# Kernel optimization log

Measured on AMD Instinct MI355X. Metric: run time of the kernel, lower is better.

## Reference

```python
import jax, jax.numpy as jnp
import numpy as np

IN_F = 4096
OUT_F = 4096
R_BLOCKS = 4
D = IN_F // R_BLOCKS          # 1024 block size
NUM_TASKS = 5
POOL = 5
EPS0 = 1e-05
SEQ = 4096


def setup_inputs() -> dict:
    key = jax.random.key(0)
    k1, k2, k3, k4 = jax.random.split(key, 4)
    return {
        "input": jax.random.normal(k1, (1, SEQ, IN_F), jnp.float32),
        "lora_route": jax.random.normal(k2, (NUM_TASKS, IN_F, POOL), jnp.float32) * 0.02,
        "lora_down": jax.random.normal(k3, (NUM_TASKS, R_BLOCKS, D, D), jnp.float32) * 0.01,
        "W": jax.random.normal(k4, (OUT_F, IN_F), jnp.float32) * 0.02,
        "task_id": 5,
    }


def _block_diag(Q):
    # Q: [r, d, d] -> [r*d, r*d] block-diagonal
    r, d, _ = Q.shape
    out = jnp.zeros((r * d, r * d), Q.dtype)
    for i in range(r):
        out = out.at[i * d:(i + 1) * d, i * d:(i + 1) * d].set(Q[i])
    return out


def reference(input, lora_route, lora_down, W, task_id):
    # eval-mode forward of OFTInjectedLinear (block_share=False, is_coft=True)
    n_tasks, in_f, pool = lora_route.shape
    r, d = lora_down.shape[1], lora_down.shape[2]
    # project_batch: eps = (eps0 * d * d) / sqrt(r)
    eps = jnp.asarray(EPS0 * d * d, input.dtype) / jnp.sqrt(jnp.asarray(r, input.dtype))

    route = lora_route[task_id - 1][None]                     # [1, in, pool]
    input_mean = jnp.mean(input, axis=1, keepdims=True)       # [1, 1, in]
    omegas = jax.nn.softmax(jnp.matmul(input_mean, route), axis=2)  # [1, 1, pool]
    omegas_mean = jnp.mean(omegas, axis=(0, 1))[:task_id]     # [task_id]
    k = min(task_id, 2)
    _, I_idx = jax.lax.top_k(omegas_mean, k)                  # selected tasks

    eye_d = jnp.eye(d, dtype=input.dtype)
    delta = jnp.eye(in_f, dtype=input.dtype)
    for i in range(k):                                        # k is a small static int
        j = I_idx[i]
        R = jnp.take(lora_down, j, axis=0)                    # [r, d, d]
        # COFT projection toward the ZERO matrix (source uses torch.zeros for I)
        nrm = jnp.sqrt(jnp.sum(R * R, axis=(1, 2), keepdims=True))  # per-block fro norm
        Rp = jnp.where(nrm <= eps, R, eps * R / jnp.maximum(nrm, 1e-12))
        # batched Cayley: Q = (I - skew) (I + skew)^{-1}
        skew = 0.5 * (Rp - jnp.swapaxes(Rp, 1, 2))
        Q = jnp.matmul(eye_d - skew, jnp.linalg.inv(eye_d + skew))  # [r, d, d]
        bd = _block_diag(Q)                                   # [in, in]
        omega_j = omegas[0, 0, j]                             # scalar (B==1)
        delta = delta * (omega_j * bd)                        # ELEMENTWISE, as in source

    filt = jnp.matmul(delta, W.T)                             # [in, out]
    return jnp.matmul(input, filt)                            # [1, S, out]
```

## Files before the change

kernel.cpp:

```cpp
#include <hip/hip_runtime.h>
#include <stdint.h>


typedef __bf16 bf16;
typedef __bf16 bf16x4 __attribute__((ext_vector_type(4)));
typedef __bf16 bf16x8 __attribute__((ext_vector_type(8)));
typedef float  f32x4  __attribute__((ext_vector_type(4)));

#define AS1 __attribute__((address_space(1)))
#define AS3 __attribute__((address_space(3)))

constexpr size_t OFF_INBF = 0;
constexpr size_t OFF_WV   = OFF_INBF + (size_t)4096 * 4096 * 2;
constexpr size_t OFF_MEAN = OFF_WV + (size_t)4096 * 4096 * 2;
constexpr size_t OFF_T    = OFF_MEAN + 4096 * 4;
constexpr size_t OFF_NRM2 = OFF_T + 8 * 1024 * 4;
constexpr size_t OFF_INFO = OFF_NRM2 + 64;
constexpr size_t OFF_V    = OFF_INFO + 64;

__global__ void mean_cvt(const float4* __restrict__ in4, float* __restrict__ meansum,
                         bf16* __restrict__ ob) {
    const int t  = threadIdx.x;
    const int f4 = blockIdx.x * 256 + t;
    const int s0 = blockIdx.y * 32;
    float sx = 0.f, sy = 0.f, sz = 0.f, sw = 0.f;
    for (int s = s0; s < s0 + 32; ++s) {
        float4 vx = in4[(size_t)s * 1024 + f4];
        sx += vx.x; sy += vx.y; sz += vx.z; sw += vx.w;
        bf16x4 bv;
        bv[0] = (bf16)vx.x; bv[1] = (bf16)vx.y; bv[2] = (bf16)vx.z; bv[3] = (bf16)vx.w;
        *(bf16x4*)&ob[(size_t)s * 4096 + f4 * 4] = bv;
    }
    atomicAdd(&meansum[f4 * 4 + 0], sx);
    atomicAdd(&meansum[f4 * 4 + 1], sy);
    atomicAdd(&meansum[f4 * 4 + 2], sz);
    atomicAdd(&meansum[f4 * 4 + 3], sw);
}

__global__ void omega_kernel(const float* __restrict__ meansum, const float* __restrict__ lora_route,
                             const int* __restrict__ task_id_p, int* __restrict__ info_i,
                             float* __restrict__ info_f) {
    __shared__ float red[256];
    __shared__ float logits[5];
    const int t = threadIdx.x;
    const int tid = task_id_p[0];
    const float* route = lora_route + (size_t)(tid - 1) * 4096 * 5;
    float acc[5] = {0.f, 0.f, 0.f, 0.f, 0.f};
    for (int f = t; f < 4096; f += 256) {
        float m = meansum[f] * (1.0f / 4096.0f);
#pragma unroll
        for (int p = 0; p < 5; ++p) acc[p] += m * route[f * 5 + p];
    }
    for (int p = 0; p < 5; ++p) {
        red[t] = acc[p];
        __syncthreads();
        for (int s = 128; s > 0; s >>= 1) {
            if (t < s) red[t] += red[t + s];
            __syncthreads();
        }
        if (t == 0) logits[p] = red[0];
        __syncthreads();
    }
    if (t == 0) {
        float mx = logits[0];
        for (int p = 1; p < 5; ++p) mx = fmaxf(mx, logits[p]);
        float e[5], se = 0.f;
        for (int p = 0; p < 5; ++p) { e[p] = expf(logits[p] - mx); se += e[p]; }
        float om[5];
        for (int p = 0; p < 5; ++p) om[p] = e[p] / se;
        const int n = tid < 5 ? tid : 5;
        int j1 = 0;
        for (int p = 1; p < n; ++p) if (om[p] > om[j1]) j1 = p;
        int j2 = -1;
        for (int p = 0; p < n; ++p) if (p != j1 && (j2 < 0 || om[p] > om[j2])) j2 = p;
        const int k = tid < 2 ? tid : 2;
        info_i[0] = j1;
        info_i[1] = (k > 1) ? j2 : j1;
        info_i[2] = k;
        float c = om[j1];
        if (k > 1) c *= om[j2];
        info_f[3] = c;
    }
}

__global__ void diag_kernel(const float* __restrict__ lora_down, const int* __restrict__ info_i,
                            float* __restrict__ T, float* __restrict__ nrm2) {
    const int bid = blockIdx.x;
    const int ts = bid >> 6;
    const int rb = (bid >> 4) & 3;
    const int a  = bid & 15;
    const int k = info_i[2];
    if (ts >= k) return;
    const int j = info_i[ts];
    const float* R = lora_down + ((size_t)(j * 4 + rb) << 20);
    __shared__ float X[64][65];
    __shared__ float Y[64][65];
    const int t = threadIdx.x;
    const int i = t >> 2, g = t & 3;
    const int a64 = a * 64;
    float tacc = 0.f, nacc = 0.f;
    for (int b = 0; b < 16; ++b) {
        __syncthreads();
#pragma unroll
        for (int qq = 0; qq < 4; ++qq) {
            const int fi = qq * 256 + t;
            const int row = fi >> 4, c4 = fi & 15;
            float4 vx = *(const float4*)&R[(size_t)(a64 + row) * 1024 + b * 64 + c4 * 4];
            X[row][c4 * 4 + 0] = vx.x; X[row][c4 * 4 + 1] = vx.y;
            X[row][c4 * 4 + 2] = vx.z; X[row][c4 * 4 + 3] = vx.w;
            nacc += vx.x * vx.x + vx.y * vx.y + vx.z * vx.z + vx.w * vx.w;
            float4 vy = *(const float4*)&R[(size_t)(b * 64 + row) * 1024 + a64 + c4 * 4];
            Y[row][c4 * 4 + 0] = vy.x; Y[row][c4 * 4 + 1] = vy.y;
            Y[row][c4 * 4 + 2] = vy.z; Y[row][c4 * 4 + 3] = vy.w;
        }
        __syncthreads();
#pragma unroll
        for (int s = 0; s < 16; ++s) {
            float xv = X[i][g * 16 + s];
            float yv = Y[g * 16 + s][i];
            float d = xv - yv;
            tacc += d * d;
        }
    }
    tacc += __shfl_xor(tacc, 1);
    tacc += __shfl_xor(tacc, 2);
    if (g == 0) T[((ts * 4 + rb) << 10) + a64 + i] = tacc;
    for (int off = 32; off > 0; off >>= 1) nacc += __shfl_down(nacc, off);
    if ((t & 63) == 0) atomicAdd(&nrm2[ts * 4 + rb], nacc);
}

__global__ void vbuild(const float* __restrict__ T, const float* __restrict__ nrm2,
                       const int* __restrict__ info_i, const float* __restrict__ info_f,
                       float* __restrict__ v) {
    const int i = blockIdx.x * 256 + threadIdx.x;
    const int k = info_i[2];
    const float c = info_f[3];
    const int rb = i >> 10, di = i & 1023;
    const float eps = 1e-5f * 1024.0f * 1024.0f / 2.0f;
    float q = c;
    for (int ts = 0; ts < k; ++ts) {
        float nrm = sqrtf(nrm2[ts * 4 + rb]);
        float scale = (nrm <= eps) ? 1.0f : eps / fmaxf(nrm, 1e-12f);
        q *= 1.0f - 0.5f * scale * scale * T[((ts * 4 + rb) << 10) + di];
    }
    v[i] = q;
}

__global__ void scaleW(const float4* __restrict__ W4, const float* __restrict__ v,
                       bf16* __restrict__ Wv) {
    const size_t stride = (size_t)gridDim.x * blockDim.x;
    for (size_t i = (size_t)blockIdx.x * blockDim.x + threadIdx.x; i < (size_t)4096 * 1024; i += stride) {
        float4 w = W4[i];
        const float* vp = &v[(i & 1023) << 2];
        bf16x4 o;
        o[0] = (bf16)(w.x * vp[0]);
        o[1] = (bf16)(w.y * vp[1]);
        o[2] = (bf16)(w.z * vp[2]);
        o[3] = (bf16)(w.w * vp[3]);
        *(bf16x4*)&Wv[i << 2] = o;
    }
}

__device__ __forceinline__ void gload_lds16(const bf16* g, bf16* lds) {
    __builtin_amdgcn_global_load_lds((const AS1 void*)g, (AS3 void*)lds, 16, 0, 0);
}

__global__ __launch_bounds__(512, 2) void gemm256(const bf16* __restrict__ A,
                                                  const bf16* __restrict__ B,
                                                  float* __restrict__ C) {
    __shared__ bf16 lds[65536];
    const int t = threadIdx.x;
    const int w = t >> 6, l = t & 63;
    const int bid = blockIdx.x;
    const int swz = ((bid & 7) << 5) | (bid >> 3);
    const int bm = swz >> 4, bn = swz & 15;
    const int wm = w >> 2, wn = w & 3;
    const int rl = l & 15, q = l >> 4;
    const int xm = (l & 7) << 4;

    const int srow = (w << 4) + (l >> 3);
    const int scol = ((l & 7) ^ (l >> 3)) << 3;
    const bf16* pA = A + (size_t)((bm << 8) + srow) * 4096 + scol;
    const bf16* pB = B + (size_t)((bn << 8) + srow) * 4096 + scol;

#define STG(dstE, srcP, h, kt) do {                                                          \
        gload_lds16((srcP) + (size_t)((h) * 128) * 4096 + (size_t)(kt) * 64,                 \
                    (bf16*)&lds[(dstE) + (h) * 8192 + w * 1024]);                            \
        gload_lds16((srcP) + (size_t)((h) * 128 + 8) * 4096 + (size_t)(kt) * 64,             \
                    (bf16*)&lds[(dstE) + (h) * 8192 + w * 1024 + 512]);                      \
    } while (0)

    const int aB = (((wm << 7) + rl) << 6);
    const int bB = 16384 + (((wn << 6) + rl) << 6);
    const int c0 = (((q << 4) + 0) ^ xm) >> 1;
    const int c1 = (((q << 4) + 64) ^ xm) >> 1;

    f32x4 acc[8][4] = {};

    STG(0, pA, 0, 0); STG(0, pA, 1, 0);
    STG(16384, pB, 0, 0); STG(16384, pB, 1, 0);
    STG(32768, pA, 0, 1); STG(32768, pA, 1, 1);

    for (int kt = 0; kt < 64; ++kt) {
        const int bufE = (kt & 1) << 15;
        const int nb = bufE ^ 32768;
        if (kt < 63) asm volatile("s_waitcnt vmcnt(4)" ::: "memory");
        else         asm volatile("s_waitcnt vmcnt(0)" ::: "memory");
        __builtin_amdgcn_s_barrier();
        asm volatile("" ::: "memory");

        bf16x8 a0[8], b0[4], a1[8], b1[4];
#pragma unroll
        for (int m = 0; m < 8; ++m) a0[m] = *(const bf16x8*)&lds[bufE + aB + m * 1024 + c0];
#pragma unroll
        for (int n = 0; n < 4; ++n) b0[n] = *(const bf16x8*)&lds[bufE + bB + n * 1024 + c0];
        if (kt + 1 < 64) STG(nb + 16384, pB, 0, kt + 1);
        __builtin_amdgcn_s_setprio(1);
#pragma unroll
        for (int m = 0; m < 4; ++m)
#pragma unroll
            for (int n = 0; n < 4; ++n)
                acc[m][n] = __builtin_amdgcn_mfma_f32_16x16x32_bf16(a0[m], b0[n], acc[m][n], 0, 0, 0);
        __builtin_amdgcn_s_setprio(0);
        __builtin_amdgcn_s_barrier();

#pragma unroll
        for (int m = 0; m < 8; ++m) a1[m] = *(const bf16x8*)&lds[bufE + aB + m * 1024 + c1];
#pragma unroll
        for (int n = 0; n < 4; ++n) b1[n] = *(const bf16x8*)&lds[bufE + bB + n * 1024 + c1];
        if (kt + 1 < 64) STG(nb + 16384, pB, 1, kt + 1);
        __builtin_amdgcn_s_setprio(1);
#pragma unroll
        for (int m = 4; m < 8; ++m)
#pragma unroll
            for (int n = 0; n < 4; ++n)
                acc[m][n] = __builtin_amdgcn_mfma_f32_16x16x32_bf16(a0[m], b0[n], acc[m][n], 0, 0, 0);
        __builtin_amdgcn_s_setprio(0);
        asm volatile("s_waitcnt lgkmcnt(0)" ::: "memory");
        __builtin_amdgcn_s_barrier();

        if (kt + 2 < 64) STG(bufE, pA, 0, kt + 2);
        __builtin_amdgcn_s_setprio(1);
#pragma unroll
        for (int m = 0; m < 4; ++m)
#pragma unroll
            for (int n = 0; n < 4; ++n)
                acc[m][n] = __builtin_amdgcn_mfma_f32_16x16x32_bf16(a1[m], b1[n], acc[m][n], 0, 0, 0);
        __builtin_amdgcn_s_setprio(0);
        __builtin_amdgcn_s_barrier();

        if (kt + 2 < 64) STG(bufE, pA, 1, kt + 2);
        __builtin_amdgcn_s_setprio(1);
#pragma unroll
        for (int m = 4; m < 8; ++m)
#pragma unroll
            for (int n = 0; n < 4; ++n)
                acc[m][n] = __builtin_amdgcn_mfma_f32_16x16x32_bf16(a1[m], b1[n], acc[m][n], 0, 0, 0);
        __builtin_amdgcn_s_setprio(0);
    }
#undef STG

    const int crow = (bm << 8) + (wm << 7) + (q << 2);
    const int ccol = (bn << 8) + (wn << 6) + rl;
#pragma unroll
    for (int m = 0; m < 8; ++m)
#pragma unroll
        for (int n = 0; n < 4; ++n)
#pragma unroll
            for (int r = 0; r < 4; ++r)
                C[(size_t)(crow + m * 16 + r) * 4096 + ccol + n * 16] = acc[m][n][r];
}

extern "C" void kernel_launch(void* const* d_in, const int* in_sizes, int n_in,
                              void* d_out, int out_size, void* d_ws, size_t ws_size,
                              hipStream_t stream) {
    const float* input      = (const float*)d_in[0];
    const float* lora_route = (const float*)d_in[1];
    const float* lora_down  = (const float*)d_in[2];
    const float* W          = (const float*)d_in[3];
    const int*   task_id    = (const int*)d_in[4];

    char* ws = (char*)d_ws;
    bf16*  inbf    = (bf16*)(ws + OFF_INBF);
    bf16*  Wv      = (bf16*)(ws + OFF_WV);
    float* meansum = (float*)(ws + OFF_MEAN);
    float* T       = (float*)(ws + OFF_T);
    float* nrm2    = (float*)(ws + OFF_NRM2);
    int*   info_i  = (int*)(ws + OFF_INFO);
    float* info_f  = (float*)(ws + OFF_INFO);
    float* v       = (float*)(ws + OFF_V);
    float* out     = (float*)d_out;

    hipMemsetAsync(ws + OFF_MEAN, 0, OFF_V + 4096 * 4 - OFF_MEAN, stream);

    mean_cvt<<<dim3(4, 128), 256, 0, stream>>>((const float4*)input, meansum, inbf);
    omega_kernel<<<1, 256, 0, stream>>>(meansum, lora_route, task_id, info_i, info_f);
    diag_kernel<<<128, 256, 0, stream>>>(lora_down, info_i, T, nrm2);
    vbuild<<<16, 256, 0, stream>>>(T, nrm2, info_i, info_f, v);
    scaleW<<<4096, 256, 0, stream>>>((const float4*)W, v, Wv);
    gemm256<<<256, 512, 0, stream>>>(inbf, Wv, out);
}
```

Measured before the change: 210.8 us.

## Widen grids for mean and diag kernels and deepen GEMM B-tile prefetch

mean_cvt now uses four times more blocks, each covering fewer sequence rows. diag_kernel is split across 2048 blocks that each handle one 64x64 tile pair and combine results with atomics. Both changes aim to fill more compute units during these memory-bound preprocessing kernels. The GEMM main loop is rescheduled so B tiles are prefetched one step further ahead, with more barriers and lgkmcnt waits interleaved to overlap LDS reads with MFMA. This adds atomic traffic and extra synchronisation, and the new vmcnt counts must match the reordered loads to stay correct.

After: 334.1 us. +58.5%, slower.

```diff
diff --git a/kernel.cpp b/kernel.cpp
--- a/kernel.cpp
+++ b/kernel.cpp
@@ -22,9 +22,9 @@
                          bf16* __restrict__ ob) {
     const int t  = threadIdx.x;
     const int f4 = blockIdx.x * 256 + t;
-    const int s0 = blockIdx.y * 32;
+    const int s0 = blockIdx.y * 8;
     float sx = 0.f, sy = 0.f, sz = 0.f, sw = 0.f;
-    for (int s = s0; s < s0 + 32; ++s) {
+    for (int s = s0; s < s0 + 8; ++s) {
         float4 vx = in4[(size_t)s * 1024 + f4];
         sx += vx.x; sy += vx.y; sz += vx.z; sw += vx.w;
         bf16x4 bv;
@@ -86,9 +86,10 @@
 __global__ void diag_kernel(const float* __restrict__ lora_down, const int* __restrict__ info_i,
                             float* __restrict__ T, float* __restrict__ nrm2) {
     const int bid = blockIdx.x;
-    const int ts = bid >> 6;
-    const int rb = (bid >> 4) & 3;
-    const int a  = bid & 15;
+    const int ts = bid >> 10;
+    const int rb = (bid >> 8) & 3;
+    const int a  = (bid >> 4) & 15;
+    const int b  = bid & 15;
     const int k = info_i[2];
     if (ts >= k) return;
     const int j = info_i[ts];
@@ -97,34 +98,30 @@
     __shared__ float Y[64][65];
     const int t = threadIdx.x;
     const int i = t >> 2, g = t & 3;
-    const int a64 = a * 64;
-    float tacc = 0.f, nacc = 0.f;
-    for (int b = 0; b < 16; ++b) {
-        __syncthreads();
-#pragma unroll
-        for (int qq = 0; qq < 4; ++qq) {
-            const int fi = qq * 256 + t;
-            const int row = fi >> 4, c4 = fi & 15;
-            float4 vx = *(const float4*)&R[(size_t)(a64 + row) * 1024 + b * 64 + c4 * 4];
-            X[row][c4 * 4 + 0] = vx.x; X[row][c4 * 4 + 1] = vx.y;
-            X[row][c4 * 4 + 2] = vx.z; X[row][c4 * 4 + 3] = vx.w;
-            nacc += vx.x * vx.x + vx.y * vx.y + vx.z * vx.z + vx.w * vx.w;
-            float4 vy = *(const float4*)&R[(size_t)(b * 64 + row) * 1024 + a64 + c4 * 4];
-            Y[row][c4 * 4 + 0] = vy.x; Y[row][c4 * 4 + 1] = vy.y;
-            Y[row][c4 * 4 + 2] = vy.z; Y[row][c4 * 4 + 3] = vy.w;
-        }
-        __syncthreads();
-#pragma unroll
-        for (int s = 0; s < 16; ++s) {
-            float xv = X[i][g * 16 + s];
-            float yv = Y[g * 16 + s][i];
-            float d = xv - yv;
-            tacc += d * d;
-        }
+    const int a64 = a * 64, b64 = b * 64;
+    float nacc = 0.f;
+#pragma unroll
+    for (int qq = 0; qq < 4; ++qq) {
+        const int fi = qq * 256 + t;
+        const int row = fi >> 4, c4 = fi & 15;
+        float4 vx = *(const float4*)&R[(size_t)(a64 + row) * 1024 + b64 + c4 * 4];
+        X[row][c4 * 4 + 0] = vx.x; X[row][c4 * 4 + 1] = vx.y;
+        X[row][c4 * 4 + 2] = vx.z; X[row][c4 * 4 + 3] = vx.w;
+        nacc += vx.x * vx.x + vx.y * vx.y + vx.z * vx.z + vx.w * vx.w;
+        float4 vy = *(const float4*)&R[(size_t)(b64 + row) * 1024 + a64 + c4 * 4];
+        Y[row][c4 * 4 + 0] = vy.x; Y[row][c4 * 4 + 1] = vy.y;
+        Y[row][c4 * 4 + 2] = vy.z; Y[row][c4 * 4 + 3] = vy.w;
+    }
+    __syncthreads();
+    float tacc = 0.f;
+#pragma unroll
+    for (int s = 0; s < 16; ++s) {
+        float d = X[i][g * 16 + s] - Y[g * 16 + s][i];
+        tacc += d * d;
     }
     tacc += __shfl_xor(tacc, 1);
     tacc += __shfl_xor(tacc, 2);
-    if (g == 0) T[((ts * 4 + rb) << 10) + a64 + i] = tacc;
+    if (g == 0) atomicAdd(&T[((ts * 4 + rb) << 10) + a64 + i], tacc);
     for (int off = 32; off > 0; off >>= 1) nacc += __shfl_down(nacc, off);
     if ((t & 63) == 0) atomicAdd(&nrm2[ts * 4 + rb], nacc);
 }
@@ -200,21 +197,25 @@
     STG(0, pA, 0, 0); STG(0, pA, 1, 0);
     STG(16384, pB, 0, 0); STG(16384, pB, 1, 0);
     STG(32768, pA, 0, 1); STG(32768, pA, 1, 1);
+    STG(32768 + 16384, pB, 0, 1);
 
     for (int kt = 0; kt < 64; ++kt) {
-        const int bufE = (kt & 1) << 15;
-        const int nb = bufE ^ 32768;
-        if (kt < 63) asm volatile("s_waitcnt vmcnt(4)" ::: "memory");
+        const int cur = (kt & 1) << 15;
+        const int nxt = cur ^ 32768;
+        if (kt < 63) asm volatile("s_waitcnt vmcnt(6)" ::: "memory");
         else         asm volatile("s_waitcnt vmcnt(0)" ::: "memory");
         __builtin_amdgcn_s_barrier();
         asm volatile("" ::: "memory");
 
-        bf16x8 a0[8], b0[4], a1[8], b1[4];
-#pragma unroll
-        for (int m = 0; m < 8; ++m) a0[m] = *(const bf16x8*)&lds[bufE + aB + m * 1024 + c0];
-#pragma unroll
-        for (int n = 0; n < 4; ++n) b0[n] = *(const bf16x8*)&lds[bufE + bB + n * 1024 + c0];
-        if (kt + 1 < 64) STG(nb + 16384, pB, 0, kt + 1);
+        bf16x8 a0[8], a1[8], b0[4], b1[4];
+#pragma unroll
+        for (int m = 0; m < 8; ++m) a0[m] = *(const bf16x8*)&lds[cur + aB + m * 1024 + c0];
+#pragma unroll
+        for (int n = 0; n < 4; ++n) b0[n] = *(const bf16x8*)&lds[cur + bB + n * 1024 + c0];
+        if (kt + 1 < 64) STG(nxt + 16384, pB, 1, kt + 1);
+        asm volatile("s_waitcnt lgkmcnt(8)" ::: "memory");
+        __builtin_amdgcn_s_barrier();
+        asm volatile("s_waitcnt lgkmcnt(0)" ::: "memory");
         __builtin_amdgcn_s_setprio(1);
 #pragma unroll
         for (int m = 0; m < 4; ++m)
@@ -225,10 +226,10 @@
         __builtin_amdgcn_s_barrier();
 
 #pragma unroll
-        for (int m = 0; m < 8; ++m) a1[m] = *(const bf16x8*)&lds[bufE + aB + m * 1024 + c1];
-#pragma unroll
-        for (int n = 0; n < 4; ++n) b1[n] = *(const bf16x8*)&lds[bufE + bB + n * 1024 + c1];
-        if (kt + 1 < 64) STG(nb + 16384, pB, 1, kt + 1);
+        for (int m = 0; m < 8; ++m) a1[m] = *(const bf16x8*)&lds[cur + aB + m * 1024 + c1];
+        asm volatile("" ::: "memory");
+        __builtin_amdgcn_s_barrier();
+        asm volatile("s_waitcnt lgkmcnt(0)" ::: "memory");
         __builtin_amdgcn_s_setprio(1);
 #pragma unroll
         for (int m = 4; m < 8; ++m)
@@ -236,10 +237,14 @@
             for (int n = 0; n < 4; ++n)
                 acc[m][n] = __builtin_amdgcn_mfma_f32_16x16x32_bf16(a0[m], b0[n], acc[m][n], 0, 0, 0);
         __builtin_amdgcn_s_setprio(0);
+        __builtin_amdgcn_s_barrier();
+
+#pragma unroll
+        for (int n = 0; n < 4; ++n) b1[n] = *(const bf16x8*)&lds[cur + bB + n * 1024 + c1];
+        if (kt + 2 < 64) STG(cur, pA, 0, kt + 2);
+        asm volatile("" ::: "memory");
+        __builtin_amdgcn_s_barrier();
         asm volatile("s_waitcnt lgkmcnt(0)" ::: "memory");
-        __builtin_amdgcn_s_barrier();
-
-        if (kt + 2 < 64) STG(bufE, pA, 0, kt + 2);
         __builtin_amdgcn_s_setprio(1);
 #pragma unroll
         for (int m = 0; m < 4; ++m)
@@ -249,7 +254,9 @@
         __builtin_amdgcn_s_setprio(0);
         __builtin_amdgcn_s_barrier();
 
-        if (kt + 2 < 64) STG(bufE, pA, 1, kt + 2);
+        if (kt + 2 < 64) { STG(cur, pA, 1, kt + 2); STG(cur + 16384, pB, 0, kt + 2); }
+        asm volatile("" ::: "memory");
+        __builtin_amdgcn_s_barrier();
         __builtin_amdgcn_s_setprio(1);
 #pragma unroll
         for (int m = 4; m < 8; ++m)
@@ -293,9 +300,9 @@
 
     hipMemsetAsync(ws + OFF_MEAN, 0, OFF_V + 4096 * 4 - OFF_MEAN, stream);
 
-    mean_cvt<<<dim3(4, 128), 256, 0, stream>>>((const float4*)input, meansum, inbf);
+    mean_cvt<<<dim3(4, 512), 256, 0, stream>>>((const float4*)input, meansum, inbf);
     omega_kernel<<<1, 256, 0, stream>>>(meansum, lora_route, task_id, info_i, info_f);
-    diag_kernel<<<128, 256, 0, stream>>>(lora_down, info_i, T, nrm2);
+    diag_kernel<<<2048, 256, 0, stream>>>(lora_down, info_i, T, nrm2);
     vbuild<<<16, 256, 0, stream>>>(T, nrm2, info_i, info_f, v);
     scaleW<<<4096, 256, 0, stream>>>((const float4*)W, v, Wv);
     gemm256<<<256, 512, 0, stream>>>(inbf, Wv, out);
```

## Split diag_kernel tile loop across blocks and reduce partials in vbuild

Applied to the files above, without the earlier changes.

diag_kernel now runs one 64x64 tile pair per block (2048 blocks) instead of looping over 16 column tiles in 128 blocks. Per-tile skew sums and Frobenius-norm partials go to a scratch area aliased onto the Wv buffer, which scaleW only writes later. vbuild sums those partials with a shared-memory tree reduction. This fills the GPU during the lora_down read phase and removes the atomics and most of the memset. In exchange, vbuild does redundant per-block norm reductions and reads 16 partials per element.

After: 202.7 us. 1.04x faster.

```diff
diff --git a/kernel.cpp b/kernel.cpp
--- a/kernel.cpp
+++ b/kernel.cpp
@@ -13,10 +13,9 @@
 constexpr size_t OFF_INBF = 0;
 constexpr size_t OFF_WV   = OFF_INBF + (size_t)4096 * 4096 * 2;
 constexpr size_t OFF_MEAN = OFF_WV + (size_t)4096 * 4096 * 2;
-constexpr size_t OFF_T    = OFF_MEAN + 4096 * 4;
-constexpr size_t OFF_NRM2 = OFF_T + 8 * 1024 * 4;
-constexpr size_t OFF_INFO = OFF_NRM2 + 64;
+constexpr size_t OFF_INFO = OFF_MEAN + 4096 * 4;
 constexpr size_t OFF_V    = OFF_INFO + 64;
+constexpr size_t TP_ELEMS = (size_t)16 * 8192;
 
 __global__ void mean_cvt(const float4* __restrict__ in4, float* __restrict__ meansum,
                          bf16* __restrict__ ob) {
@@ -84,64 +83,80 @@
 }
 
 __global__ void diag_kernel(const float* __restrict__ lora_down, const int* __restrict__ info_i,
-                            float* __restrict__ T, float* __restrict__ nrm2) {
+                            float* __restrict__ TP, float* __restrict__ NP) {
     const int bid = blockIdx.x;
-    const int ts = bid >> 6;
-    const int rb = (bid >> 4) & 3;
-    const int a  = bid & 15;
+    const int ts = bid >> 10;
+    const int rb = (bid >> 8) & 3;
+    const int a  = (bid >> 4) & 15;
+    const int b  = bid & 15;
     const int k = info_i[2];
     if (ts >= k) return;
     const int j = info_i[ts];
     const float* R = lora_down + ((size_t)(j * 4 + rb) << 20);
     __shared__ float X[64][65];
     __shared__ float Y[64][65];
+    __shared__ float wsum[4];
     const int t = threadIdx.x;
     const int i = t >> 2, g = t & 3;
-    const int a64 = a * 64;
-    float tacc = 0.f, nacc = 0.f;
-    for (int b = 0; b < 16; ++b) {
-        __syncthreads();
-#pragma unroll
-        for (int qq = 0; qq < 4; ++qq) {
-            const int fi = qq * 256 + t;
-            const int row = fi >> 4, c4 = fi & 15;
-            float4 vx = *(const float4*)&R[(size_t)(a64 + row) * 1024 + b * 64 + c4 * 4];
-            X[row][c4 * 4 + 0] = vx.x; X[row][c4 * 4 + 1] = vx.y;
-            X[row][c4 * 4 + 2] = vx.z; X[row][c4 * 4 + 3] = vx.w;
-            nacc += vx.x * vx.x + vx.y * vx.y + vx.z * vx.z + vx.w * vx.w;
-            float4 vy = *(const float4*)&R[(size_t)(b * 64 + row) * 1024 + a64 + c4 * 4];
-            Y[row][c4 * 4 + 0] = vy.x; Y[row][c4 * 4 + 1] = vy.y;
-            Y[row][c4 * 4 + 2] = vy.z; Y[row][c4 * 4 + 3] = vy.w;
-        }
-        __syncthreads();
-#pragma unroll
-        for (int s = 0; s < 16; ++s) {
-            float xv = X[i][g * 16 + s];
-            float yv = Y[g * 16 + s][i];
-            float d = xv - yv;
-            tacc += d * d;
-        }
+    const int a64 = a * 64, b64 = b * 64;
+    float nacc = 0.f;
+#pragma unroll
+    for (int qq = 0; qq < 4; ++qq) {
+        const int fi = qq * 256 + t;
+        const int row = fi >> 4, c4 = fi & 15;
+        float4 vx = *(const float4*)&R[(size_t)(a64 + row) * 1024 + b64 + c4 * 4];
+        X[row][c4 * 4 + 0] = vx.x; X[row][c4 * 4 + 1] = vx.y;
+        X[row][c4 * 4 + 2] = vx.z; X[row][c4 * 4 + 3] = vx.w;
+        nacc += vx.x * vx.x + vx.y * vx.y + vx.z * vx.z + vx.w * vx.w;
+        float4 vy = *(const float4*)&R[(size_t)(b64 + row) * 1024 + a64 + c4 * 4];
+        Y[row][c4 * 4 + 0] = vy.x; Y[row][c4 * 4 + 1] = vy.y;
+        Y[row][c4 * 4 + 2] = vy.z; Y[row][c4 * 4 + 3] = vy.w;
+    }
+    __syncthreads();
+    float tacc = 0.f;
+#pragma unroll
+    for (int s = 0; s < 16; ++s) {
+        float d = X[i][g * 16 + s] - Y[g * 16 + s][i];
+        tacc += d * d;
     }
     tacc += __shfl_xor(tacc, 1);
     tacc += __shfl_xor(tacc, 2);
-    if (g == 0) T[((ts * 4 + rb) << 10) + a64 + i] = tacc;
+    if (g == 0) TP[b * 8192 + ((ts * 4 + rb) << 10) + a64 + i] = tacc;
     for (int off = 32; off > 0; off >>= 1) nacc += __shfl_down(nacc, off);
-    if ((t & 63) == 0) atomicAdd(&nrm2[ts * 4 + rb], nacc);
-}
-
-__global__ void vbuild(const float* __restrict__ T, const float* __restrict__ nrm2,
+    if ((t & 63) == 0) wsum[t >> 6] = nacc;
+    __syncthreads();
+    if (t == 0) NP[(ts * 4 + rb) * 256 + a * 16 + b] = wsum[0] + wsum[1] + wsum[2] + wsum[3];
+}
+
+__global__ void vbuild(const float* __restrict__ TP, const float* __restrict__ NP,
                        const int* __restrict__ info_i, const float* __restrict__ info_f,
                        float* __restrict__ v) {
-    const int i = blockIdx.x * 256 + threadIdx.x;
+    __shared__ float red[256];
+    __shared__ float snrm[8];
+    const int t = threadIdx.x;
+    for (int g = 0; g < 8; ++g) {
+        red[t] = NP[g * 256 + t];
+        __syncthreads();
+        for (int s = 128; s > 0; s >>= 1) {
+            if (t < s) red[t] += red[t + s];
+            __syncthreads();
+        }
+        if (t == 0) snrm[g] = red[0];
+        __syncthreads();
+    }
+    const int i = blockIdx.x * 256 + t;
     const int k = info_i[2];
     const float c = info_f[3];
     const int rb = i >> 10, di = i & 1023;
     const float eps = 1e-5f * 1024.0f * 1024.0f / 2.0f;
     float q = c;
     for (int ts = 0; ts < k; ++ts) {
-        float nrm = sqrtf(nrm2[ts * 4 + rb]);
+        float tt = 0.f;
+#pragma unroll
+        for (int bb = 0; bb < 16; ++bb) tt += TP[bb * 8192 + ((ts * 4 + rb) << 10) + di];
+        float nrm = sqrtf(snrm[ts * 4 + rb]);
         float scale = (nrm <= eps) ? 1.0f : eps / fmaxf(nrm, 1e-12f);
-        q *= 1.0f - 0.5f * scale * scale * T[((ts * 4 + rb) << 10) + di];
+        q *= 1.0f - 0.5f * scale * scale * tt;
     }
     v[i] = q;
 }
@@ -284,19 +299,19 @@
     bf16*  inbf    = (bf16*)(ws + OFF_INBF);
     bf16*  Wv      = (bf16*)(ws + OFF_WV);
     float* meansum = (float*)(ws + OFF_MEAN);
-    float* T       = (float*)(ws + OFF_T);
-    float* nrm2    = (float*)(ws + OFF_NRM2);
     int*   info_i  = (int*)(ws + OFF_INFO);
     float* info_f  = (float*)(ws + OFF_INFO);
     float* v       = (float*)(ws + OFF_V);
+    float* TP      = (float*)(ws + OFF_WV);
+    float* NP      = TP + TP_ELEMS;
     float* out     = (float*)d_out;
 
-    hipMemsetAsync(ws + OFF_MEAN, 0, OFF_V + 4096 * 4 - OFF_MEAN, stream);
+    hipMemsetAsync(meansum, 0, 4096 * 4, stream);
 
     mean_cvt<<<dim3(4, 128), 256, 0, stream>>>((const float4*)input, meansum, inbf);
     omega_kernel<<<1, 256, 0, stream>>>(meansum, lora_route, task_id, info_i, info_f);
-    diag_kernel<<<128, 256, 0, stream>>>(lora_down, info_i, T, nrm2);
-    vbuild<<<16, 256, 0, stream>>>(T, nrm2, info_i, info_f, v);
+    diag_kernel<<<2048, 256, 0, stream>>>(lora_down, info_i, TP, NP);
+    vbuild<<<16, 256, 0, stream>>>(TP, NP, info_i, info_f, v);
     scaleW<<<4096, 256, 0, stream>>>((const float4*)W, v, Wv);
     gemm256<<<256, 512, 0, stream>>>(inbf, Wv, out);
 }
```
